# Kernel optimization log

Measured on AMD Instinct MI355X. Metric: run time of the kernel, lower is better.

The kernel has to match this reference:

```python
import jax, jax.numpy as jnp
import numpy as np

LN_EPS = 1e-5
LOCAL_SIZE = 256
N_HEAD, D_HEAD = 16, 64


def layer_norm_c(x):
    # layer norm over channel dim (axis=1), no affine params (matches F.layer_norm(x.T,(d,)).T)
    m = jnp.mean(x, axis=1, keepdims=True)
    v = jnp.var(x, axis=1, keepdims=True)
    return (x - m) / jnp.sqrt(v + LN_EPS)


def rel_shift(x):
    # x: [b, n, q, k] -> Transformer-XL relative shift
    b, n, q, k = x.shape
    x = jnp.pad(x, ((0, 0), (0, 0), (0, 0), (1, 0)))
    return x.reshape(b, n, k + 1, q)[:, :, 1:].reshape(b, n, q, k)


def setup_inputs() -> dict:
    key = jax.random.key(0)
    ks = jax.random.split(key, 14)
    bsz, d_model, qlen, mlen = 4, 1024, 512, 512
    klen = qlen + mlen
    d_inner = 4096
    s = lambda k, shape, sc=0.05: jax.random.normal(k, shape, dtype=jnp.float32) * sc
    return {
        "z1ss": jax.random.normal(ks[0], (bsz, d_model, qlen), dtype=jnp.float32),
        "uss": jax.random.normal(ks[1], (bsz, 3 * d_model, klen), dtype=jnp.float32) * 0.1,
        "z0": jax.random.normal(ks[2], (bsz, d_model, mlen), dtype=jnp.float32),
        "pos_emb": jax.random.normal(ks[3], (1, d_model, klen), dtype=jnp.float32),
        "qkv_w": s(ks[4], (3 * d_model, d_model)),
        "r_w": s(ks[5], (d_model, d_model)),
        "r_w_bias": s(ks[6], (N_HEAD, D_HEAD)),
        "r_r_bias": s(ks[7], (N_HEAD, D_HEAD)),
        "o_w": s(ks[8], (d_model, d_model)),
        "o_b": s(ks[9], (d_model,)),
        "ff1_w": s(ks[10], (d_inner, d_model)),
        "ff1_b": s(ks[11], (d_inner,)),
        "ff2_w": s(ks[12], (d_model, d_inner)),
        "ff2_b": s(ks[13], (d_model,)),
    }


def reference(z1ss, uss, z0, pos_emb, qkv_w, r_w, r_w_bias, r_r_bias, o_w, o_b,
              ff1_w, ff1_b, ff2_w, ff2_b):
    bsz, d_model, qlen = z1ss.shape
    mlen = z0.shape[2]
    n_head, d_head = N_HEAD, D_HEAD
    scale = 1.0 / d_head ** 0.5

    # ---- self-attention (post-lnorm path) ----
    cat = jnp.concatenate([z0, z1ss], axis=-1)              # [b, d, klen]
    klen = cat.shape[2]
    w_heads = jnp.einsum('od,bdk->bok', qkv_w, cat) + uss   # [b, 3d, klen]
    r_head_k = jnp.einsum('od,dk->ok', r_w, pos_emb[0])     # [d, rlen]
    rlen = r_head_k.shape[1]

    w_head_q, w_head_k, w_head_v = jnp.split(w_heads, 3, axis=1)
    w_head_q = w_head_q[:, :, -qlen:]
    w_head_q = w_head_q.reshape(bsz, n_head, d_head, qlen)
    w_head_k = w_head_k.reshape(bsz, n_head, d_head, klen)
    w_head_v = w_head_v.reshape(bsz, n_head, d_head, klen)
    r_head_k = r_head_k.reshape(n_head, d_head, rlen)

    rw_q = w_head_q + r_w_bias[:, :, None]                  # [b,n,d,q]
    AC = jnp.einsum('bndi,bndj->bnij', rw_q, w_head_k)      # [b,n,q,k]
    rr_q = w_head_q + r_r_bias[:, :, None]
    BD = rel_shift(jnp.einsum('bndi,ndj->bnij', rr_q, r_head_k))
    attn_score = (AC + BD) * scale

    local_size = LOCAL_SIZE if LOCAL_SIZE else 1000
    i = jnp.arange(qlen)[:, None]
    j = jnp.arange(klen)[None, :]
    mask = (j > i + mlen) | (j <= i + mlen - local_size)    # causal + local window
    attn_score = jnp.where(mask[None, None], -jnp.inf, attn_score)

    attn_prob = jax.nn.softmax(attn_score, axis=-1)
    attn_vec = jnp.einsum('bnij,bndj->bndi', attn_prob, w_head_v)
    attn_vec = attn_vec.reshape(bsz, n_head * d_head, qlen)
    attn_out = jnp.einsum('od,bdq->boq', o_w, attn_vec) + o_b[None, :, None]
    x = layer_norm_c(attn_out + z1ss)                       # post-lnorm

    # ---- position-wise FF (weight-shared, post-lnorm) ----
    h = jax.nn.relu(jnp.einsum('id,bdq->biq', ff1_w, x) + ff1_b[None, :, None])
    out2 = jnp.einsum('di,biq->bdq', ff2_w, h) + ff2_b[None, :, None]
    return layer_norm_c(out2 + x)
```

## Files before the change

### kernel.cpp

```cpp
#include <hip/hip_runtime.h>
#include <hip/hip_bf16.h>

typedef unsigned short u16;
typedef __attribute__((ext_vector_type(8))) short s8v;
typedef __attribute__((ext_vector_type(4))) short s4v;
typedef __attribute__((ext_vector_type(4))) float f4v;

__device__ __forceinline__ float s2f(u16 s) {
    unsigned int u = ((unsigned int)s) << 16;
    return __builtin_bit_cast(float, u);
}
__device__ __forceinline__ u16 f2s(float f) {
    __hip_bfloat16 h = __float2bfloat16(f);
    return __builtin_bit_cast(u16, h);
}

__device__ __forceinline__ void gl2lds16(const u16* g, u16* l) {
    __builtin_amdgcn_global_load_lds((const __attribute__((address_space(1))) void*)g,
                                     (__attribute__((address_space(3))) void*)l, 16, 0, 0);
}

#define BSZ 4
#define DM 1024
#define QLEN 512
#define MLEN 512
#define KLEN 1024
#define DI 4096
#define NH 16
#define DH 64
#define WIN 256

#define CONV_BLKS 13312
#define Z0_BLKS 2048
#define Z1_BLKS 2048
#define POS_BLKS 256
__global__ __launch_bounds__(256) void prep(
    const float* __restrict__ qkv_w, const float* __restrict__ r_w,
    const float* __restrict__ o_w, const float* __restrict__ ff1_w,
    const float* __restrict__ ff2_w,
    u16* __restrict__ wQ, u16* __restrict__ wR, u16* __restrict__ wO,
    u16* __restrict__ wF1, u16* __restrict__ wF2,
    const float* __restrict__ z0, const float* __restrict__ z1ss,
    const float* __restrict__ pos,
    u16* __restrict__ catT, u16* __restrict__ posT)
{
    int bx = blockIdx.x, tid = threadIdx.x;
    if (bx < CONV_BLKS) {
        const int e0 = 786432, e1 = e0 + 262144, e2 = e1 + 262144, e3 = e2 + 1048576;
        int i = bx * 256 + tid;
        const float* s; u16* d; int off;
        if (i < e0)      { s = qkv_w; d = wQ;  off = i; }
        else if (i < e1) { s = r_w;   d = wR;  off = i - e0; }
        else if (i < e2) { s = o_w;   d = wO;  off = i - e1; }
        else if (i < e3) { s = ff1_w; d = wF1; off = i - e2; }
        else             { s = ff2_w; d = wF2; off = i - e3; }
        f4v v = *(const f4v*)&s[(size_t)off * 4];
        s4v o;
#pragma unroll
        for (int k = 0; k < 4; ++k) o[k] = (short)f2s(v[k]);
        *(s4v*)&d[(size_t)off * 4] = o;
        return;
    }
    __shared__ float tile[32][33];
    int tx = tid & 31, ty = tid >> 5;
    const float* src; u16* dst; long sS, sD; int ldS, ldD, colOff, rowOff, t0, f0, b;
    if (bx < CONV_BLKS + Z0_BLKS) {
        int idx = bx - CONV_BLKS;
        t0 = (idx & 15) * 32; f0 = ((idx >> 4) & 31) * 32; b = idx >> 9;
        src = z0;   sS = (long)DM * MLEN; ldS = MLEN; colOff = 0;
        dst = catT; sD = (long)KLEN * DM; ldD = DM;  rowOff = 0;
    } else if (bx < CONV_BLKS + Z0_BLKS + Z1_BLKS) {
        int idx = bx - CONV_BLKS - Z0_BLKS;
        t0 = (idx & 15) * 32; f0 = ((idx >> 4) & 31) * 32; b = idx >> 9;
        src = z1ss; sS = (long)DM * QLEN; ldS = QLEN; colOff = 0;
        dst = catT; sD = (long)KLEN * DM; ldD = DM;  rowOff = MLEN;
    } else {
        int idx = bx - CONV_BLKS - Z0_BLKS - Z1_BLKS;
        t0 = (idx & 7) * 32; f0 = (idx >> 3) * 32; b = 0;
        src = pos;  sS = 0; ldS = KLEN; colOff = KLEN - WIN;
        dst = posT; sD = 0; ldD = DM;   rowOff = 0;
    }
#pragma unroll
    for (int p = 0; p < 4; ++p)
        tile[ty + 8 * p][tx] = src[(size_t)b * sS + (size_t)(f0 + ty + 8 * p) * ldS + colOff + t0 + tx];
    __syncthreads();
#pragma unroll
    for (int p = 0; p < 4; ++p)
        dst[(size_t)b * sD + (size_t)(rowOff + t0 + ty + 8 * p) * ldD + f0 + tx] = f2s(tile[tx][ty + 8 * p]);
}

__global__ __launch_bounds__(256) void uss_add(
    const float* __restrict__ uss, u16* __restrict__ whT, u16* __restrict__ vT)
{
    __shared__ float tile[32][33];
    int b = blockIdx.z;
    int t0 = blockIdx.x * 32, fy = blockIdx.y;
    int tx = threadIdx.x, ty = threadIdx.y;
    if (fy < 32 && t0 < 512) return;
    const float* S = uss + (size_t)b * 3072 * 1024;
    if (fy < 64) {
        int f0 = fy * 32;
        u16* D = whT + (size_t)b * 1024 * 3072;
#pragma unroll
        for (int p = 0; p < 4; ++p)
            tile[ty + 8 * p][tx] = S[(size_t)(f0 + ty + 8 * p) * 1024 + t0 + tx];
        __syncthreads();
#pragma unroll
        for (int p = 0; p < 4; ++p) {
            size_t o = (size_t)(t0 + ty + 8 * p) * 3072 + f0 + tx;
            D[o] = f2s(s2f(D[o]) + tile[tx][ty + 8 * p]);
        }
    } else {
        int d0 = (fy - 64) * 32;
#pragma unroll
        for (int p = 0; p < 4; ++p) {
            int d = d0 + ty + 8 * p;
            size_t ui = ((size_t)2048 + d) * 1024 + t0 + tx;
            size_t vi = (size_t)d * 4096 + (size_t)b * KLEN + t0 + tx;
            vT[vi] = f2s(s2f(vT[vi]) + S[ui]);
        }
    }
}

__global__ __launch_bounds__(256) void trans_b2f(
    const u16* __restrict__ src, long sS, int ldS,
    float* __restrict__ dst, long sD, int ldD)
{
    __shared__ float tile[32][33];
    int b = blockIdx.z;
    int t0 = blockIdx.x * 32, f0 = blockIdx.y * 32;
    int tx = threadIdx.x, ty = threadIdx.y;
#pragma unroll
    for (int p = 0; p < 4; ++p)
        tile[ty + 8 * p][tx] = s2f(src[(size_t)b * sS + (size_t)(f0 + ty + 8 * p) * ldS + t0 + tx]);
    __syncthreads();
#pragma unroll
    for (int p = 0; p < 4; ++p)
        dst[(size_t)b * sD + (size_t)(t0 + ty + 8 * p) * ldD + f0 + tx] = tile[tx][ty + 8 * p];
}

template<int BN, int SPLIT>
__global__ __launch_bounds__(256) void gemm_bt(
    const u16* __restrict__ A,
    const u16* __restrict__ B,
    u16* __restrict__ C,
    float* __restrict__ fOut,
    int M, int K,
    const float* __restrict__ bias,
    int relu,
    int qskip,
    long pstride,
    u16* __restrict__ vTout)
{
    constexpr int BM = 128, BK = 64;
    constexpr int MI = (BN == 128) ? 4 : 2;
    constexpr int NI = 4;
    const int n0 = blockIdx.x * BN, m0 = blockIdx.y * BM;
    if (qskip && m0 + BM <= 1024 && (n0 & 1023) < 512) return;
    const int Ks = K / SPLIT;
    const int kbeg = blockIdx.z * Ks;
    __shared__ __align__(16) u16 As[BM * BK];
    __shared__ __align__(16) u16 Bs[BN * BK];
    const int tid = threadIdx.x, lane = tid & 63, wv = tid >> 6;
    const int l15 = lane & 15, quad = lane >> 4;
    const int wm = (BN == 128) ? (wv >> 1) * 64 : wv * 32;
    const int wn = (BN == 128) ? (wv & 1) * 64 : 0;
    f4v acc[MI][NI] = {};
    for (int kk = kbeg; kk < kbeg + Ks; kk += BK) {
        __syncthreads();
#pragma unroll
        for (int p = 0; p < (BM * 8) / 256; ++p) {
            int c = p * 256 + tid, r = c >> 3, q = c & 7, qs = q ^ (r & 7);
            gl2lds16(&A[(size_t)(m0 + r) * K + kk + qs * 8], &As[c * 8]);
        }
#pragma unroll
        for (int p = 0; p < (BN * 8) / 256; ++p) {
            int c = p * 256 + tid, r = c >> 3, q = c & 7, qs = q ^ (r & 7);
            gl2lds16(&B[(size_t)(n0 + r) * K + kk + qs * 8], &Bs[c * 8]);
        }
        __syncthreads();
#pragma unroll
        for (int k0 = 0; k0 < BK; k0 += 32) {
            s8v af[MI], bf[NI];
#pragma unroll
            for (int mi = 0; mi < MI; ++mi) {
                int r = wm + mi * 16 + l15;
                af[mi] = *(const s8v*)&As[r * BK + ((((k0 >> 3) + quad) ^ (r & 7)) << 3)];
            }
#pragma unroll
            for (int ni = 0; ni < NI; ++ni) {
                int r = wn + ni * 16 + l15;
                bf[ni] = *(const s8v*)&Bs[r * BK + ((((k0 >> 3) + quad) ^ (r & 7)) << 3)];
            }
#pragma unroll
            for (int mi = 0; mi < MI; ++mi)
#pragma unroll
                for (int ni = 0; ni < NI; ++ni)
                    acc[mi][ni] = __builtin_amdgcn_mfma_f32_16x16x32_bf16(af[mi], bf[ni], acc[mi][ni], 0, 0, 0);
        }
    }
    if (SPLIT > 1) {
        float* base = fOut + (long)blockIdx.z * pstride;
#pragma unroll
        for (int mi = 0; mi < MI; ++mi) {
            int m = m0 + wm + mi * 16 + quad * 4;
#pragma unroll
            for (int ni = 0; ni < NI; ++ni) {
                int n = n0 + wn + ni * 16 + l15;
                *(f4v*)&base[(size_t)n * M + m] = acc[mi][ni];
            }
        }
    } else if (vTout && m0 >= 2048) {
#pragma unroll
        for (int mi = 0; mi < MI; ++mi) {
            int m = m0 + wm + mi * 16 + quad * 4;
#pragma unroll
            for (int ni = 0; ni < NI; ++ni) {
                int n = n0 + wn + ni * 16 + l15;
#pragma unroll
                for (int r2 = 0; r2 < 4; ++r2)
                    vTout[(size_t)(m + r2 - 2048) * 4096 + n] = f2s(acc[mi][ni][r2]);
            }
        }
    } else {
#pragma unroll
        for (int mi = 0; mi < MI; ++mi) {
            int m = m0 + wm + mi * 16 + quad * 4;
            float bv[4] = {0.f, 0.f, 0.f, 0.f};
            if (bias) {
#pragma unroll
                for (int r2 = 0; r2 < 4; ++r2) bv[r2] = bias[m + r2];
            }
#pragma unroll
            for (int ni = 0; ni < NI; ++ni) {
                int n = n0 + wn + ni * 16 + l15;
                float o[4];
#pragma unroll
                for (int r2 = 0; r2 < 4; ++r2) o[r2] = acc[mi][ni][r2] + bv[r2];
                if (relu) {
#pragma unroll
                    for (int r2 = 0; r2 < 4; ++r2) o[r2] = fmaxf(o[r2], 0.f);
                }
                s4v st;
#pragma unroll
                for (int r2 = 0; r2 < 4; ++r2) st[r2] = (short)f2s(o[r2]);
                *(s4v*)&C[(size_t)n * M + m] = st;
            }
        }
    }
}

#define QT 64
#define SROW 260
__global__ __launch_bounds__(256, 2) void attn_mfma(
    const u16* __restrict__ WHT,
    const u16* __restrict__ VT,
    const u16* __restrict__ RT,
    const float* __restrict__ rwb, const float* __restrict__ rrb,
    u16* __restrict__ avT)
{
    __shared__ __align__(16) float sS[QT * SROW];

    const int qt = blockIdx.x, n = blockIdx.y, b = blockIdx.z;
    const int i0 = qt * QT, j0 = i0 + WIN + 1;
    const int tid = threadIdx.x, lane = tid & 63, wv = tid >> 6;
    const int l15 = lane & 15, quad = lane >> 4;
    const u16* W = WHT + (size_t)b * KLEN * (3 * DM);

    s8v qac[4][2], qbd[4][2];
#pragma unroll
    for (int h = 0; h < 4; ++h) {
        int qrow = MLEN + i0 + 16 * h + l15;
#pragma unroll
        for (int kc = 0; kc < 2; ++kc) {
            int col = n * DH + kc * 32 + quad * 8;
            s8v qv = *(const s8v*)&W[(size_t)qrow * (3 * DM) + col];
            s8v a, c;
#pragma unroll
            for (int e = 0; e < 8; ++e) {
                float qf = s2f((u16)qv[e]);
                a[e] = (short)f2s(qf + rwb[col + e]);
                c[e] = (short)f2s(qf + rrb[col + e]);
            }
            qac[h][kc] = a; qbd[h][kc] = c;
        }
    }

    for (int ci = wv; ci < 20; ci += 4) {
        int j = j0 + ci * 16 + l15; if (j > KLEN - 1) j = KLEN - 1;
        const u16* Kr = &W[(size_t)j * (3 * DM) + DM + n * DH + quad * 8];
        s8v k0 = *(const s8v*)Kr, k1 = *(const s8v*)(Kr + 32);
#pragma unroll
        for (int h = 0; h < 4; ++h) {
            f4v acc = {};
            acc = __builtin_amdgcn_mfma_f32_16x16x32_bf16(qac[h][0], k0, acc, 0, 0, 0);
            acc = __builtin_amdgcn_mfma_f32_16x16x32_bf16(qac[h][1], k1, acc, 0, 0, 0);
#pragma unroll
            for (int r2 = 0; r2 < 4; ++r2) {
                int qi = 16 * h + quad * 4 + r2;
                int t = ci * 16 + l15 - qi;
                if ((unsigned)t < 256u) sS[qi * SROW + t] = acc[r2];
            }
        }
    }
    __syncthreads();

#pragma unroll
    for (int cc = 0; cc < 4; ++cc) {
        int ci = wv + cc * 4;
        const u16* Rr = &RT[(size_t)(ci * 16 + l15) * DM + n * DH + quad * 8];
        s8v r0 = *(const s8v*)Rr, r1 = *(const s8v*)(Rr + 32);
#pragma unroll
        for (int h = 0; h < 4; ++h) {
            f4v acc = {};
            acc = __builtin_amdgcn_mfma_f32_16x16x32_bf16(qbd[h][0], r0, acc, 0, 0, 0);
            acc = __builtin_amdgcn_mfma_f32_16x16x32_bf16(qbd[h][1], r1, acc, 0, 0, 0);
#pragma unroll
            for (int r2 = 0; r2 < 4; ++r2) {
                int qi = 16 * h + quad * 4 + r2;
                sS[qi * SROW + ci * 16 + l15] += acc[r2];
            }
        }
    }
    __syncthreads();

    {
        int g = tid >> 4, l = tid & 15;
#pragma unroll
        for (int h = 0; h < 4; ++h) {
            int r = g + 16 * h;
            float vals[16], mx = -1e30f;
#pragma unroll
            for (int k = 0; k < 16; ++k) {
                float s = sS[r * SROW + l + 16 * k] * 0.125f;
                vals[k] = s; mx = fmaxf(mx, s);
            }
            asm volatile("" ::: "memory");
#pragma unroll
            for (int d = 1; d < 16; d <<= 1) mx = fmaxf(mx, __shfl_xor(mx, d, 16));
            float sum = 0.f;
#pragma unroll
            for (int k = 0; k < 16; ++k) { vals[k] = __expf(vals[k] - mx); sum += vals[k]; }
#pragma unroll
            for (int d = 1; d < 16; d <<= 1) sum += __shfl_xor(sum, d, 16);
            float inv = 1.f / sum;
            u16* sPr = (u16*)&sS[r * SROW];
#pragma unroll
            for (int k = 0; k < 16; ++k) sPr[r + 1 + l + 16 * k] = f2s(vals[k] * inv);
            for (int p = l; p <= r; p += 16) sPr[p] = 0;
            for (int p = r + 257 + l; p < 320; p += 16) sPr[p] = 0;
        }
    }
    __syncthreads();

    const u16* sPu = (const u16*)sS;
    const size_t vbase = (size_t)(n * DH + wv * 16 + l15) * 4096
                       + (size_t)b * KLEN + (j0 - 1) + quad * 8;
    f4v o[4] = {};
#pragma unroll
    for (int kc = 0; kc < 10; ++kc) {
        s8v bb = *(const s8v*)&VT[vbase + kc * 32];
#pragma unroll
        for (int h = 0; h < 4; ++h) {
            s8v a = *(const s8v*)&sPu[(size_t)(16 * h + l15) * (2 * SROW) + kc * 32 + quad * 8];
            o[h] = __builtin_amdgcn_mfma_f32_16x16x32_bf16(a, bb, o[h], 0, 0, 0);
        }
    }
#pragma unroll
    for (int h = 0; h < 4; ++h)
#pragma unroll
        for (int r2 = 0; r2 < 4; ++r2) {
            int qi = quad * 4 + r2;
            avT[((size_t)b * QLEN + i0 + 16 * h + qi) * DM + n * DH + wv * 16 + l15] = f2s(o[h][r2]);
        }
}

__global__ __launch_bounds__(256) void ln_f(
    const float* __restrict__ P, long pstride, int nparts,
    const float* __restrict__ bias,
    const u16* __restrict__ res, int resMode, u16* __restrict__ out)
{
    int n = blockIdx.x, tid = threadIdx.x;
    int lane = tid & 63, wv = tid >> 6;
    int f = tid * 4;
    int rrow = resMode ? (((n >> 9) * 2 + 1) * 512 + (n & 511)) : n;
    f4v pv = *(const f4v*)&P[(size_t)n * DM + f];
    for (int p = 1; p < nparts; ++p) {
        const float* Pp = P + (long)p * pstride;
        pv += *(const f4v*)&Pp[(size_t)n * DM + f];
    }
    s4v rv = *(const s4v*)&res[(size_t)rrow * DM + f];
    f4v bv = *(const f4v*)&bias[f];
    float v[4];
#pragma unroll
    for (int k = 0; k < 4; ++k) v[k] = pv[k] + bv[k] + s2f((u16)rv[k]);
    float s = v[0] + v[1] + v[2] + v[3];
    float ss = v[0] * v[0] + v[1] * v[1] + v[2] * v[2] + v[3] * v[3];
#pragma unroll
    for (int d = 1; d < 64; d <<= 1) {
        s += __shfl_xor(s, d, 64);
        ss += __shfl_xor(ss, d, 64);
    }
    __shared__ float ps[4], pss[4];
    if (lane == 0) { ps[wv] = s; pss[wv] = ss; }
    __syncthreads();
    float S = ps[0] + ps[1] + ps[2] + ps[3];
    float SS = pss[0] + pss[1] + pss[2] + pss[3];
    float m = S * (1.f / DM);
    float var = SS * (1.f / DM) - m * m;
    float inv = rsqrtf(fmaxf(var, 0.f) + 1e-5f);
    s4v st;
#pragma unroll
    for (int k = 0; k < 4; ++k) st[k] = (short)f2s((v[k] - m) * inv);
    *(s4v*)&out[(size_t)n * DM + f] = st;
}

extern "C" void kernel_launch(void* const* d_in, const int* in_sizes, int n_in,
                              void* d_out, int out_size, void* d_ws, size_t ws_size,
                              hipStream_t stream) {
    const float* z1ss  = (const float*)d_in[0];
    const float* uss   = (const float*)d_in[1];
    const float* z0    = (const float*)d_in[2];
    const float* pos   = (const float*)d_in[3];
    const float* qkv_w = (const float*)d_in[4];
    const float* r_w   = (const float*)d_in[5];
    const float* rwb   = (const float*)d_in[6];
    const float* rrb   = (const float*)d_in[7];
    const float* o_w   = (const float*)d_in[8];
    const float* o_b   = (const float*)d_in[9];
    const float* ff1_w = (const float*)d_in[10];
    const float* ff1_b = (const float*)d_in[11];
    const float* ff2_w = (const float*)d_in[12];
    const float* ff2_b = (const float*)d_in[13];

    u16* ws = (u16*)d_ws;
    u16* wQ   = ws;
    u16* wR   = ws + 3145728;
    u16* wO   = ws + 4194304;
    u16* wF1  = ws + 5242880;
    u16* wF2  = ws + 9437184;
    u16* catT = ws + 13631488;
    u16* whT  = ws + 17825792;
    u16* posT = ws + 30408704;
    u16* rT   = ws + 30670848;
    u16* avT  = ws + 30932992;
    u16* xT   = ws + 33030144;
    float* pref = (float*)(ws + 35127296);
    u16* hT   = whT;
    u16* outT = catT;

    u16* vT = (u16*)pref;

    float* part1 = (float*)d_ws;
    long pstr = part1 - pref;

    dim3 tblk(32, 8);

    prep<<<CONV_BLKS + Z0_BLKS + Z1_BLKS + POS_BLKS, 256, 0, stream>>>(
        qkv_w, r_w, o_w, ff1_w, ff2_w, wQ, wR, wO, wF1, wF2,
        z0, z1ss, pos, catT, posT);

    gemm_bt<64, 1><<<dim3(64, 24, 1), 256, 0, stream>>>(
        wQ, catT, whT, nullptr, 3 * DM, DM, nullptr, 0, 1, 0, vT);

    uss_add<<<dim3(32, 96, BSZ), tblk, 0, stream>>>(uss, whT, vT);

    gemm_bt<64, 1><<<dim3(4, 8, 1), 256, 0, stream>>>(
        wR, posT, rT, nullptr, DM, DM, nullptr, 0, 0, 0, nullptr);

    attn_mfma<<<dim3(QLEN / QT, NH, BSZ), 256, 0, stream>>>(whT, vT, rT, rwb, rrb, avT);

    gemm_bt<64, 2><<<dim3(32, 8, 2), 256, 0, stream>>>(
        wO, avT, nullptr, pref, DM, DM, nullptr, 0, 0, pstr, nullptr);

    ln_f<<<2048, 256, 0, stream>>>(pref, pstr, 2, o_b, catT, 1, xT);

    gemm_bt<64, 1><<<dim3(32, 32, 1), 256, 0, stream>>>(
        wF1, xT, hT, nullptr, DI, DM, ff1_b, 1, 0, 0, nullptr);

    gemm_bt<64, 2><<<dim3(32, 8, 2), 256, 0, stream>>>(
        wF2, hT, nullptr, pref, DM, DI, nullptr, 0, 0, pstr, nullptr);

    ln_f<<<2048, 256, 0, stream>>>(pref, pstr, 2, ff2_b, xT, 0, outT);

    trans_b2f<<<dim3(32, 16, BSZ), tblk, 0, stream>>>(outT, (long)QLEN * DM, DM,
                                                      (float*)d_out, (long)DM * QLEN, QLEN);
}
```

Before: 325.9 us.

## Fuse R-projection into QKV GEMM, split FF2 4-way, fuse final LN with transpose

The position projection GEMM now runs as an extra row of blocks inside the QKV GEMM launch, which removes one tiny launch. The FF2 GEMM is split four ways along K into four fp32 partial buffers to put more blocks in flight. A new ln_out kernel sums the partials, adds bias and residual, applies layer norm and writes the transposed fp32 output directly, replacing the separate ln_f and trans_b2f kernels. In exchange there is more partial-sum memory traffic and a strided transposed store in the final kernel.

```diff
diff --git a/kernel.cpp b/kernel.cpp
--- a/kernel.cpp
+++ b/kernel.cpp
@@ -122,23 +122,6 @@
     }
 }
 
-__global__ __launch_bounds__(256) void trans_b2f(
-    const u16* __restrict__ src, long sS, int ldS,
-    float* __restrict__ dst, long sD, int ldD)
-{
-    __shared__ float tile[32][33];
-    int b = blockIdx.z;
-    int t0 = blockIdx.x * 32, f0 = blockIdx.y * 32;
-    int tx = threadIdx.x, ty = threadIdx.y;
-#pragma unroll
-    for (int p = 0; p < 4; ++p)
-        tile[ty + 8 * p][tx] = s2f(src[(size_t)b * sS + (size_t)(f0 + ty + 8 * p) * ldS + t0 + tx]);
-    __syncthreads();
-#pragma unroll
-    for (int p = 0; p < 4; ++p)
-        dst[(size_t)b * sD + (size_t)(t0 + ty + 8 * p) * ldD + f0 + tx] = tile[tx][ty + 8 * p];
-}
-
 template<int BN, int SPLIT>
 __global__ __launch_bounds__(256) void gemm_bt(
     const u16* __restrict__ A,
@@ -150,13 +133,30 @@
     int relu,
     int qskip,
     long pstride,
-    u16* __restrict__ vTout)
+    u16* __restrict__ vTout,
+    const u16* __restrict__ A2,
+    const u16* __restrict__ B2,
+    u16* __restrict__ C2,
+    float* __restrict__ fOut2,
+    long pstride2)
 {
     constexpr int BM = 128, BK = 64;
     constexpr int MI = (BN == 128) ? 4 : 2;
     constexpr int NI = 4;
-    const int n0 = blockIdx.x * BN, m0 = blockIdx.y * BM;
-    if (qskip && m0 + BM <= 1024 && (n0 & 1023) < 512) return;
+    int n0, m0, Mv;
+    const u16* Ap; const u16* Bp; u16* Cp;
+    bool isR = false;
+    if (A2 && blockIdx.y == gridDim.y - 1) {
+        if (blockIdx.x >= 32) return;
+        isR = true;
+        n0 = (blockIdx.x & 3) * BN;
+        m0 = (blockIdx.x >> 2) * BM;
+        Ap = A2; Bp = B2; Cp = C2; Mv = 1024;
+    } else {
+        n0 = blockIdx.x * BN; m0 = blockIdx.y * BM;
+        if (qskip && m0 + BM <= 1024 && (n0 & 1023) < 512) return;
+        Ap = A; Bp = B; Cp = C; Mv = M;
+    }
     const int Ks = K / SPLIT;
     const int kbeg = blockIdx.z * Ks;
     __shared__ __align__(16) u16 As[BM * BK];
@@ -171,12 +171,12 @@
 #pragma unroll
         for (int p = 0; p < (BM * 8) / 256; ++p) {
             int c = p * 256 + tid, r = c >> 3, q = c & 7, qs = q ^ (r & 7);
-            gl2lds16(&A[(size_t)(m0 + r) * K + kk + qs * 8], &As[c * 8]);
+            gl2lds16(&Ap[(size_t)(m0 + r) * K + kk + qs * 8], &As[c * 8]);
         }
 #pragma unroll
         for (int p = 0; p < (BN * 8) / 256; ++p) {
             int c = p * 256 + tid, r = c >> 3, q = c & 7, qs = q ^ (r & 7);
-            gl2lds16(&B[(size_t)(n0 + r) * K + kk + qs * 8], &Bs[c * 8]);
+            gl2lds16(&Bp[(size_t)(n0 + r) * K + kk + qs * 8], &Bs[c * 8]);
         }
         __syncthreads();
 #pragma unroll
@@ -200,17 +200,19 @@
         }
     }
     if (SPLIT > 1) {
-        float* base = fOut + (long)blockIdx.z * pstride;
+        int z = blockIdx.z;
+        float* base = (z < 2) ? fOut + (long)z * pstride
+                              : fOut2 + (long)(z - 2) * pstride2;
 #pragma unroll
         for (int mi = 0; mi < MI; ++mi) {
             int m = m0 + wm + mi * 16 + quad * 4;
 #pragma unroll
             for (int ni = 0; ni < NI; ++ni) {
                 int n = n0 + wn + ni * 16 + l15;
-                *(f4v*)&base[(size_t)n * M + m] = acc[mi][ni];
-            }
-        }
-    } else if (vTout && m0 >= 2048) {
+                *(f4v*)&base[(size_t)n * Mv + m] = acc[mi][ni];
+            }
+        }
+    } else if (vTout && !isR && m0 >= 2048) {
 #pragma unroll
         for (int mi = 0; mi < MI; ++mi) {
             int m = m0 + wm + mi * 16 + quad * 4;
@@ -227,7 +229,7 @@
         for (int mi = 0; mi < MI; ++mi) {
             int m = m0 + wm + mi * 16 + quad * 4;
             float bv[4] = {0.f, 0.f, 0.f, 0.f};
-            if (bias) {
+            if (bias && !isR) {
 #pragma unroll
                 for (int r2 = 0; r2 < 4; ++r2) bv[r2] = bias[m + r2];
             }
@@ -237,14 +239,14 @@
                 float o[4];
 #pragma unroll
                 for (int r2 = 0; r2 < 4; ++r2) o[r2] = acc[mi][ni][r2] + bv[r2];
-                if (relu) {
+                if (relu && !isR) {
 #pragma unroll
                     for (int r2 = 0; r2 < 4; ++r2) o[r2] = fmaxf(o[r2], 0.f);
                 }
                 s4v st;
 #pragma unroll
                 for (int r2 = 0; r2 < 4; ++r2) st[r2] = (short)f2s(o[r2]);
-                *(s4v*)&C[(size_t)n * M + m] = st;
+                *(s4v*)&Cp[(size_t)n * Mv + m] = st;
             }
         }
     }
@@ -413,6 +415,58 @@
 #pragma unroll
     for (int k = 0; k < 4; ++k) st[k] = (short)f2s((v[k] - m) * inv);
     *(s4v*)&out[(size_t)n * DM + f] = st;
+}
+
+#define LNR 16
+#define LROW 1030
+__global__ __launch_bounds__(256) void ln_out(
+    const float* __restrict__ P0, const float* __restrict__ P1,
+    const float* __restrict__ P2, const float* __restrict__ P3,
+    const float* __restrict__ bias, const u16* __restrict__ res,
+    float* __restrict__ out)
+{
+    __shared__ float rows[LNR * LROW];
+    __shared__ float sm[LNR], si[LNR];
+    int n0 = blockIdx.x * LNR;
+    int tid = threadIdx.x;
+    int r = tid >> 4, l = tid & 15;
+    int n = n0 + r;
+    float s = 0.f, ss = 0.f;
+    for (int k = 0; k < 16; ++k) {
+        int f = (l + 16 * k) * 4;
+        f4v v = *(const f4v*)&P0[(size_t)n * DM + f];
+        v += *(const f4v*)&P1[(size_t)n * DM + f];
+        v += *(const f4v*)&P2[(size_t)n * DM + f];
+        v += *(const f4v*)&P3[(size_t)n * DM + f];
+        s4v rv = *(const s4v*)&res[(size_t)n * DM + f];
+        f4v bv = *(const f4v*)&bias[f];
+        float* dst = &rows[r * LROW + f];
+#pragma unroll
+        for (int j = 0; j < 4; ++j) {
+            float x = v[j] + bv[j] + s2f((u16)rv[j]);
+            dst[j] = x;
+            s += x; ss += x * x;
+        }
+    }
+#pragma unroll
+    for (int d = 1; d < 16; d <<= 1) {
+        s += __shfl_xor(s, d, 16);
+        ss += __shfl_xor(ss, d, 16);
+    }
+    if (l == 0) {
+        float m = s * (1.f / DM);
+        float var = ss * (1.f / DM) - m * m;
+        sm[r] = m; si[r] = rsqrtf(fmaxf(var, 0.f) + 1e-5f);
+    }
+    __syncthreads();
+    int b = n0 >> 9, q0 = n0 & 511;
+    int qi = tid & 15, g = tid >> 4;
+    float m = sm[qi], inv = si[qi];
+    float* O = out + (size_t)b * DM * QLEN + q0 + qi;
+    for (int k = 0; k < 64; ++k) {
+        int f = g + 16 * k;
+        O[(size_t)f * QLEN] = (rows[qi * LROW + f] - m) * inv;
+    }
 }
 
 extern "C" void kernel_launch(void* const* d_in, const int* in_sizes, int n_in,
@@ -447,12 +501,14 @@
     u16* xT   = ws + 33030144;
     float* pref = (float*)(ws + 35127296);
     u16* hT   = whT;
-    u16* outT = catT;
 
     u16* vT = (u16*)pref;
 
     float* part1 = (float*)d_ws;
-    long pstr = part1 - pref;
+    float* part2 = (float*)(ws + 4194304);
+    float* part3 = (float*)catT;
+    long pstr  = part1 - pref;
+    long pstr2 = part3 - part2;
 
     dim3 tblk(32, 8);
 
@@ -460,29 +516,28 @@
         qkv_w, r_w, o_w, ff1_w, ff2_w, wQ, wR, wO, wF1, wF2,
         z0, z1ss, pos, catT, posT);
 
-    gemm_bt<64, 1><<<dim3(64, 24, 1), 256, 0, stream>>>(
-        wQ, catT, whT, nullptr, 3 * DM, DM, nullptr, 0, 1, 0, vT);
+    gemm_bt<64, 1><<<dim3(64, 25, 1), 256, 0, stream>>>(
+        wQ, catT, whT, nullptr, 3 * DM, DM, nullptr, 0, 1, 0, vT,
+        wR, posT, rT, nullptr, 0);
 
     uss_add<<<dim3(32, 96, BSZ), tblk, 0, stream>>>(uss, whT, vT);
 
-    gemm_bt<64, 1><<<dim3(4, 8, 1), 256, 0, stream>>>(
-        wR, posT, rT, nullptr, DM, DM, nullptr, 0, 0, 0, nullptr);
-
     attn_mfma<<<dim3(QLEN / QT, NH, BSZ), 256, 0, stream>>>(whT, vT, rT, rwb, rrb, avT);
 
     gemm_bt<64, 2><<<dim3(32, 8, 2), 256, 0, stream>>>(
-        wO, avT, nullptr, pref, DM, DM, nullptr, 0, 0, pstr, nullptr);
+        wO, avT, nullptr, pref, DM, DM, nullptr, 0, 0, pstr, nullptr,
+        nullptr, nullptr, nullptr, nullptr, 0);
 
     ln_f<<<2048, 256, 0, stream>>>(pref, pstr, 2, o_b, catT, 1, xT);
 
     gemm_bt<64, 1><<<dim3(32, 32, 1), 256, 0, stream>>>(
-        wF1, xT, hT, nullptr, DI, DM, ff1_b, 1, 0, 0, nullptr);
-
-    gemm_bt<64, 2><<<dim3(32, 8, 2), 256, 0, stream>>>(
-        wF2, hT, nullptr, pref, DM, DI, nullptr, 0, 0, pstr, nullptr);
-
-    ln_f<<<2048, 256, 0, stream>>>(pref, pstr, 2, ff2_b, xT, 0, outT);
-
-    trans_b2f<<<dim3(32, 16, BSZ), tblk, 0, stream>>>(outT, (long)QLEN * DM, DM,
-                                                      (float*)d_out, (long)DM * QLEN, QLEN);
-}
+        wF1, xT, hT, nullptr, DI, DM, ff1_b, 1, 0, 0, nullptr,
+        nullptr, nullptr, nullptr, nullptr, 0);
+
+    gemm_bt<64, 4><<<dim3(32, 8, 4), 256, 0, stream>>>(
+        wF2, hT, nullptr, pref, DM, DI, nullptr, 0, 0, pstr, nullptr,
+        nullptr, nullptr, nullptr, part2, pstr2);
+
+    ln_out<<<2048 / LNR, 256, 0, stream>>>(
+        pref, part1, part2, part3, ff2_b, xT, (float*)d_out);
+}
```

After: 318.5 us. -2.3%, faster.
